# Kernel optimization log

Measured on AMD Instinct MI355X. Metric: run time of the kernel, lower is better.

The kernel has to match this reference:

```python
import jax, jax.numpy as jnp
import numpy as np

SCALE = 8.0  # sqrt(d_k), d_k = 64
NEG_INF = -1000000000.0


def setup_inputs() -> dict:
    key = jax.random.key(0)
    ks = jax.random.split(key, 7)
    B, H, S, D = 2, 8, 4096, 64
    shp = (B, H, S, D)
    q_a = jax.random.normal(ks[0], shp, dtype=jnp.float32)
    k_a = jax.random.normal(ks[1], shp, dtype=jnp.float32)
    v_a = jax.random.normal(ks[2], shp, dtype=jnp.float32)
    q_s = jax.random.normal(ks[3], shp, dtype=jnp.float32)
    k_s = jax.random.normal(ks[4], shp, dtype=jnp.float32)
    v_s = jax.random.normal(ks[5], shp, dtype=jnp.float32)
    mask = jax.random.randint(ks[6], (B, 1, 1, S), 0, 2, dtype=jnp.int32)
    return {"q_a": q_a, "k_a": k_a, "v_a": v_a,
            "q_s": q_s, "k_s": k_s, "v_s": v_s, "mask": mask}


def reference(q_a, k_a, v_a, q_s, k_s, v_s, mask):
    # a2a + a2s + s2a + s2s == (q_a + q_s) @ (k_a + k_s)^T  (exact algebra)
    q = q_a + q_s                               # [B,H,S,D]
    k = k_a + k_s                               # [B,H,S,D]
    score = jnp.einsum("bhqd,bhkd->bhqk", q, k) / SCALE  # [B,H,S,S]
    score = jnp.where(mask == 0, NEG_INF, score)
    attn = jax.nn.softmax(score, axis=-1)       # dropout p=0 (eval/identity)
    out = jnp.einsum("bhqk,bhkd->bhqd", attn, v_a + v_s)
    return out
```

## Files before the change

### kernel.cpp

```cpp
#include <hip/hip_runtime.h>
#include <hip/hip_bf16.h>

#define S_   4096
#define D_   64
#define BH_  16
#define QW   64
#define QBLK 256
#define KVB  128
#define NCH  2

typedef __attribute__((ext_vector_type(8)))  short short8_t;
typedef __attribute__((ext_vector_type(16))) float f32x16;
#define QSCALE 0.18033688011112042f

__device__ __forceinline__ unsigned short f2bf(float f) {
  unsigned u = __float_as_uint(f);
  u += 0x7fffu + ((u >> 16) & 1u);
  return (unsigned short)(u >> 16);
}

__device__ __forceinline__ void glds16(const unsigned short* g, unsigned short* l) {
  __builtin_amdgcn_global_load_lds(
      (const __attribute__((address_space(1))) unsigned int*)g,
      (__attribute__((address_space(3))) unsigned int*)l, 16, 0, 0);
}

__global__ void addcvt2_kernel(const float* __restrict__ a, const float* __restrict__ b,
                               unsigned short* __restrict__ o, float scale, int n) {
  int i = (blockIdx.x * blockDim.x + threadIdx.x) * 4;
  if (i >= n) return;
  float4 x = *(const float4*)(a + i);
  float4 y = *(const float4*)(b + i);
  ushort4 r;
  r.x = f2bf((x.x + y.x) * scale); r.y = f2bf((x.y + y.y) * scale);
  r.z = f2bf((x.z + y.z) * scale); r.w = f2bf((x.w + y.w) * scale);
  *(ushort4*)(o + i) = r;
}

__global__ void compact_kernel(const int* __restrict__ mask, int* __restrict__ idx,
                               int* __restrict__ cnt) {
  __shared__ int ps[256];
  int b = blockIdx.x, tid = threadIdx.x;
  const int* mb = mask + (size_t)b * S_;
  int m[16], c = 0;
  int base = tid * 16;
#pragma unroll
  for (int i = 0; i < 16; ++i) { m[i] = mb[base + i]; c += (m[i] != 0); }
  ps[tid] = c;
  __syncthreads();
  for (int off = 1; off < 256; off <<= 1) {
    int add = (tid >= off) ? ps[tid - off] : 0;
    __syncthreads();
    ps[tid] += add;
    __syncthreads();
  }
  int pos = ps[tid] - c;
#pragma unroll
  for (int i = 0; i < 16; ++i) if (m[i]) idx[(size_t)b * S_ + pos++] = base + i;
  if (tid == 255) cnt[b] = ps[255];
}

__global__ void kvgather_kernel(const float* __restrict__ ka, const float* __restrict__ ks,
                                const float* __restrict__ va, const float* __restrict__ vs,
                                const int* __restrict__ idx, const int* __restrict__ cnt,
                                unsigned short* __restrict__ khat,
                                unsigned short* __restrict__ vt) {
  __shared__ __align__(16) unsigned short t[D_][72];
  int bh = blockIdx.y, b = bh >> 3;
  int s0 = blockIdx.x * 64;
  int C = cnt[b];
  int tid = threadIdx.x;
  int row16 = tid >> 4;
  int col4  = (tid & 15) * 4;
#pragma unroll
  for (int p = 0; p < 4; ++p) {
    int srow = p * 16 + row16;
    int j = s0 + srow;
    float4 xv = {0, 0, 0, 0}, yv = {0, 0, 0, 0};
    float4 xk = {0, 0, 0, 0}, yk = {0, 0, 0, 0};
    if (j < C) {
      int src = idx[(size_t)b * S_ + j];
      size_t off = ((size_t)bh * S_ + src) * D_ + col4;
      xv = *(const float4*)(va + off);
      yv = *(const float4*)(vs + off);
      xk = *(const float4*)(ka + off);
      yk = *(const float4*)(ks + off);
    }
    t[col4 + 0][srow] = f2bf(xv.x + yv.x);
    t[col4 + 1][srow] = f2bf(xv.y + yv.y);
    t[col4 + 2][srow] = f2bf(xv.z + yv.z);
    t[col4 + 3][srow] = f2bf(xv.w + yv.w);
    ushort4 rk;
    rk.x = f2bf(xk.x + yk.x); rk.y = f2bf(xk.y + yk.y);
    rk.z = f2bf(xk.z + yk.z); rk.w = f2bf(xk.w + yk.w);
    *(ushort4*)(khat + ((size_t)bh * S_ + j) * D_ + col4) = rk;
  }
  __syncthreads();
#pragma unroll
  for (int r = 0; r < 2; ++r) {
    int e = (r * 256 + tid) * 8;
    int d = e >> 6, sc = e & 63;
    short8_t v = *(const short8_t*)&t[d][sc];
    *(short8_t*)(vt + ((size_t)bh * D_ + d) * S_ + s0 + sc) = v;
  }
}

__global__ __launch_bounds__(256, 2) void attn_kernel(
    const unsigned short* __restrict__ Qb, const unsigned short* __restrict__ Kb,
    const unsigned short* __restrict__ Vt, const int* __restrict__ cnt,
    float* __restrict__ out, float* __restrict__ Opar, float2* __restrict__ Ml) {
  __shared__ __align__(16) unsigned short lK[2][KVB * 64];
  __shared__ __align__(16) unsigned short lV[2][64 * KVB];

  const int tid  = threadIdx.x;
  const int wave = tid >> 6;
  const int lane = tid & 63;
  const int l31  = lane & 31;
  const int h5   = lane >> 5;
  const int rsw  = l31 & 7;
  const int bh   = blockIdx.y;
  const int ch   = blockIdx.z;
  const int qrow0 = blockIdx.x * QBLK + wave * QW + l31;
  const int b    = bh >> 3;
  const int C    = cnt[b];
  const int NTt  = (C + KVB - 1) / KVB;
  const int tpc  = (NTt + NCH - 1) / NCH;
  const int ts   = ch * tpc;
  const int te   = (ts + tpc < NTt) ? (ts + tpc) : NTt;

  short8_t qf[2][4];
#pragma unroll
  for (int qb = 0; qb < 2; ++qb) {
    const unsigned short* qp = Qb + ((size_t)bh * S_ + qrow0 + 32 * qb) * D_ + h5 * 8;
#pragma unroll
    for (int t4 = 0; t4 < 4; ++t4) qf[qb][t4] = *(const short8_t*)(qp + t4 * 16);
  }

  const unsigned short* gk0 = Kb + (size_t)bh * S_ * D_;
  const unsigned short* gv0 = Vt + (size_t)bh * D_ * S_;

  int srcK[4], srcV[4], ldsB[4];
#pragma unroll
  for (int r2 = 0; r2 < 4; ++r2) {
    int c = r2 * 256 + tid;
    int rowK = c >> 3, gK = (c & 7) ^ (rowK & 7);
    srcK[r2] = rowK * 64 + gK * 8;
    int rowV = c >> 4, gg = c & 15;
    int swg = (gg & 8) | ((gg & 7) ^ (rowV & 7));
    srcV[r2] = rowV * S_ + swg * 8;
    ldsB[r2] = r2 * 2048 + wave * 512;
  }

  f32x16 acc0[2], acc1[2];
  float mrow[2], lrow[2];
#pragma unroll
  for (int qb = 0; qb < 2; ++qb) {
    acc0[qb] = (f32x16)(0.0f); acc1[qb] = (f32x16)(0.0f);
    mrow[qb] = -1e30f; lrow[qb] = 0.0f;
  }

  if (ts < te) {
#pragma unroll
    for (int r2 = 0; r2 < 4; ++r2) {
      glds16(gk0 + (size_t)ts * KVB * D_ + srcK[r2], &lK[0][ldsB[r2]]);
      glds16(gv0 + ts * KVB + srcV[r2], &lV[0][ldsB[r2]]);
    }

    for (int t = ts; t < te; ++t) {
      const int cur = (t - ts) & 1;
      if (t + 1 < te) {
#pragma unroll
        for (int r2 = 0; r2 < 4; ++r2) {
          glds16(gk0 + (size_t)(t + 1) * KVB * D_ + srcK[r2], &lK[cur ^ 1][ldsB[r2]]);
          glds16(gv0 + (t + 1) * KVB + srcV[r2], &lV[cur ^ 1][ldsB[r2]]);
        }
        asm volatile("s_waitcnt vmcnt(8)" ::: "memory");
      } else {
        asm volatile("s_waitcnt vmcnt(0)" ::: "memory");
      }
      __builtin_amdgcn_s_barrier();
      __builtin_amdgcn_sched_barrier(0);

#pragma unroll
      for (int h = 0; h < 2; ++h) {
        f32x16 sv0[2], sv1[2];
#pragma unroll
        for (int qb = 0; qb < 2; ++qb) { sv0[qb] = (f32x16)(0.0f); sv1[qb] = (f32x16)(0.0f); }
        __builtin_amdgcn_s_setprio(1);
#pragma unroll
        for (int t4 = 0; t4 < 4; ++t4) {
          int g = ((2 * t4 + h5) ^ rsw) * 8;
          short8_t kf0 = *(const short8_t*)&lK[cur][(h * 64 + l31) * 64 + g];
          short8_t kf1 = *(const short8_t*)&lK[cur][(h * 64 + 32 + l31) * 64 + g];
          sv0[0] = __builtin_amdgcn_mfma_f32_32x32x16_bf16(kf0, qf[0][t4], sv0[0], 0, 0, 0);
          sv0[1] = __builtin_amdgcn_mfma_f32_32x32x16_bf16(kf0, qf[1][t4], sv0[1], 0, 0, 0);
          sv1[0] = __builtin_amdgcn_mfma_f32_32x32x16_bf16(kf1, qf[0][t4], sv1[0], 0, 0, 0);
          sv1[1] = __builtin_amdgcn_mfma_f32_32x32x16_bf16(kf1, qf[1][t4], sv1[1], 0, 0, 0);
        }
        __builtin_amdgcn_s_setprio(0);

        if (t == NTt - 1) {
          int kvb = t * KVB + h * 64;
#pragma unroll
          for (int i = 0; i < 16; ++i) {
            int key = kvb + (i & 3) + 8 * (i >> 2) + 4 * h5;
#pragma unroll
            for (int qb = 0; qb < 2; ++qb) {
              if (key >= C) sv0[qb][i] = -1e9f;
              if (key + 32 >= C) sv1[qb][i] = -1e9f;
            }
          }
        }

        unsigned int pkw[2][16];
#pragma unroll
        for (int qb = 0; qb < 2; ++qb) {
          float tmx[8];
#pragma unroll
          for (int i = 0; i < 8; ++i)
            tmx[i] = fmaxf(fmaxf(sv0[qb][i], sv0[qb][i + 8]),
                           fmaxf(sv1[qb][i], sv1[qb][i + 8]));
#pragma unroll
          for (int i = 0; i < 4; ++i) tmx[i] = fmaxf(tmx[i], tmx[i + 4]);
          float tm = fmaxf(fmaxf(tmx[0], tmx[1]), fmaxf(tmx[2], tmx[3]));
          tm = fmaxf(tm, __shfl_xor(tm, 32));

          if (__any(tm > mrow[qb] + 8.0f)) {
            float mnew = fmaxf(mrow[qb], tm);
            float sc = __builtin_amdgcn_exp2f(mrow[qb] - mnew);
            mrow[qb] = mnew;
            lrow[qb] *= sc;
#pragma unroll
            for (int i = 0; i < 16; ++i) { acc0[qb][i] *= sc; acc1[qb][i] *= sc; }
          }

          float m = mrow[qb];
          float t0 = 0.f, t1 = 0.f, t2 = 0.f, t3 = 0.f;
#pragma unroll
          for (int i = 0; i < 16; i += 4) {
            sv0[qb][i + 0] = __builtin_amdgcn_exp2f(sv0[qb][i + 0] - m); t0 += sv0[qb][i + 0];
            sv0[qb][i + 1] = __builtin_amdgcn_exp2f(sv0[qb][i + 1] - m); t1 += sv0[qb][i + 1];
            sv0[qb][i + 2] = __builtin_amdgcn_exp2f(sv0[qb][i + 2] - m); t2 += sv0[qb][i + 2];
            sv0[qb][i + 3] = __builtin_amdgcn_exp2f(sv0[qb][i + 3] - m); t3 += sv0[qb][i + 3];
            sv1[qb][i + 0] = __builtin_amdgcn_exp2f(sv1[qb][i + 0] - m); t0 += sv1[qb][i + 0];
            sv1[qb][i + 1] = __builtin_amdgcn_exp2f(sv1[qb][i + 1] - m); t1 += sv1[qb][i + 1];
            sv1[qb][i + 2] = __builtin_amdgcn_exp2f(sv1[qb][i + 2] - m); t2 += sv1[qb][i + 2];
            sv1[qb][i + 3] = __builtin_amdgcn_exp2f(sv1[qb][i + 3] - m); t3 += sv1[qb][i + 3];
          }
          float tsum = (t0 + t1) + (t2 + t3);
          tsum += __shfl_xor(tsum, 32);
          lrow[qb] += tsum;

#pragma unroll
          for (int rg = 0; rg < 4; ++rg) {
            __hip_bfloat162 a0 = __float22bfloat162_rn({sv0[qb][rg * 4 + 0], sv0[qb][rg * 4 + 1]});
            __hip_bfloat162 a1 = __float22bfloat162_rn({sv0[qb][rg * 4 + 2], sv0[qb][rg * 4 + 3]});
            __hip_bfloat162 b0 = __float22bfloat162_rn({sv1[qb][rg * 4 + 0], sv1[qb][rg * 4 + 1]});
            __hip_bfloat162 b1 = __float22bfloat162_rn({sv1[qb][rg * 4 + 2], sv1[qb][rg * 4 + 3]});
            pkw[qb][rg * 2 + 0] = *(unsigned int*)&a0;
            pkw[qb][rg * 2 + 1] = *(unsigned int*)&a1;
            pkw[qb][8 + rg * 2 + 0] = *(unsigned int*)&b0;
            pkw[qb][8 + rg * 2 + 1] = *(unsigned int*)&b1;
          }
        }

        __builtin_amdgcn_s_setprio(1);
#pragma unroll
        for (int kt = 0; kt < 4; ++kt) {
          const int n = kt >> 1, k1 = kt & 1;
          int gcol = ((h * 8) | ((2 * kt + h5) ^ rsw)) * 8;
          short8_t vf0 = *(const short8_t*)&lV[cur][l31 * KVB + gcol];
          short8_t vf1 = *(const short8_t*)&lV[cur][(32 + l31) * KVB + gcol];
#pragma unroll
          for (int qb = 0; qb < 2; ++qb) {
            unsigned int sA = pkw[qb][n * 8 + (2 * k1 + h5) * 2 + 0];
            unsigned int sB = pkw[qb][n * 8 + (2 * k1 + h5) * 2 + 1];
            unsigned int xA = pkw[qb][n * 8 + (2 * k1 + (h5 ^ 1)) * 2 + 0];
            unsigned int xB = pkw[qb][n * 8 + (2 * k1 + (h5 ^ 1)) * 2 + 1];
            unsigned int pA = (unsigned int)__shfl_xor((int)xA, 32);
            unsigned int pB = (unsigned int)__shfl_xor((int)xB, 32);
            union { unsigned int u[4]; short8_t v; } bb;
            bb.u[0] = h5 ? pA : sA;
            bb.u[1] = h5 ? pB : sB;
            bb.u[2] = h5 ? sA : pA;
            bb.u[3] = h5 ? sB : pB;
            acc0[qb] = __builtin_amdgcn_mfma_f32_32x32x16_bf16(vf0, bb.v, acc0[qb], 0, 0, 0);
            acc1[qb] = __builtin_amdgcn_mfma_f32_32x32x16_bf16(vf1, bb.v, acc1[qb], 0, 0, 0);
          }
        }
        __builtin_amdgcn_s_setprio(0);
      }

      __builtin_amdgcn_sched_barrier(0);
      __builtin_amdgcn_s_barrier();
    }
  }

  float* Op = (ch == 0) ? out : Opar;
#pragma unroll
  for (int qb = 0; qb < 2; ++qb) {
    float* op = Op + ((size_t)bh * S_ + qrow0 + 32 * qb) * D_;
#pragma unroll
    for (int rg = 0; rg < 4; ++rg) {
      float4 o0, o1;
      o0.x = acc0[qb][rg * 4 + 0]; o0.y = acc0[qb][rg * 4 + 1];
      o0.z = acc0[qb][rg * 4 + 2]; o0.w = acc0[qb][rg * 4 + 3];
      o1.x = acc1[qb][rg * 4 + 0]; o1.y = acc1[qb][rg * 4 + 1];
      o1.z = acc1[qb][rg * 4 + 2]; o1.w = acc1[qb][rg * 4 + 3];
      *(float4*)(op + rg * 8 + h5 * 4) = o0;
      *(float4*)(op + 32 + rg * 8 + h5 * 4) = o1;
    }
    if (h5 == 0) {
      float2 st; st.x = mrow[qb]; st.y = lrow[qb];
      Ml[(size_t)ch * (BH_ * S_) + (size_t)bh * S_ + qrow0 + 32 * qb] = st;
    }
  }
}

__global__ void combine_kernel(const float* __restrict__ O1, const float2* __restrict__ Ml,
                               float* __restrict__ out) {
  int gid = blockIdx.x * 256 + threadIdx.x;
  int row = gid >> 2, qd = (gid & 3) * 16;
  float2 a = Ml[row];
  float2 b = Ml[BH_ * S_ + row];
  float M = fmaxf(a.x, b.x);
  float w0 = exp2f(a.x - M), w1 = exp2f(b.x - M);
  float inv = 1.0f / (a.y * w0 + b.y * w1);
  w0 *= inv; w1 *= inv;
  const float4* p0 = (const float4*)(out + (size_t)row * D_ + qd);
  const float4* p1 = (const float4*)(O1 + (size_t)row * D_ + qd);
  float4* po = (float4*)(out + (size_t)row * D_ + qd);
#pragma unroll
  for (int i = 0; i < 4; ++i) {
    float4 x = p0[i], y = p1[i];
    float4 r;
    r.x = x.x * w0 + y.x * w1; r.y = x.y * w0 + y.y * w1;
    r.z = x.z * w0 + y.z * w1; r.w = x.w * w0 + y.w * w1;
    po[i] = r;
  }
}

extern "C" void kernel_launch(void* const* d_in, const int* in_sizes, int n_in,
                              void* d_out, int out_size, void* d_ws, size_t ws_size,
                              hipStream_t stream) {
  const float* q_a = (const float*)d_in[0];
  const float* k_a = (const float*)d_in[1];
  const float* v_a = (const float*)d_in[2];
  const float* q_s = (const float*)d_in[3];
  const float* k_s = (const float*)d_in[4];
  const float* v_s = (const float*)d_in[5];
  const int*   mask = (const int*)d_in[6];
  float* out = (float*)d_out;
  (void)in_sizes; (void)n_in; (void)out_size; (void)ws_size;

  const int N = BH_ * S_ * D_;
  unsigned short* qb   = (unsigned short*)d_ws;
  unsigned short* khat = qb + N;
  unsigned short* vt   = khat + N;
  int*  idx  = (int*)(vt + N);
  int*  cnt  = idx + 2 * S_;
  float* O1  = (float*)(cnt + 4);
  float2* ml = (float2*)(O1 + N);

  compact_kernel<<<2, 256, 0, stream>>>(mask, idx, cnt);
  addcvt2_kernel<<<N / 1024, 256, 0, stream>>>(q_a, q_s, qb, QSCALE, N);
  {
    dim3 g(S_ / 64, BH_);
    kvgather_kernel<<<g, 256, 0, stream>>>(k_a, k_s, v_a, v_s, idx, cnt, khat, vt);
  }
  {
    dim3 g(S_ / QBLK, BH_, NCH);
    attn_kernel<<<g, 256, 0, stream>>>(qb, khat, vt, cnt, out, O1, ml);
  }
  combine_kernel<<<(BH_ * S_ * 4) / 256, 256, 0, stream>>>(O1, ml, out);
}
```

Baseline: 126.3 us.

## Fuse mask compaction into KV gather and Q add-convert into attention

Drops the separate compact kernel: every kvgather block now recomputes the mask prefix scan itself and keeps only its 64-entry slice of source indices in LDS. Also drops the Q add/scale/bf16-convert kernel: the attention kernel reads q_a and q_s in fp32 and builds its bf16 Q fragments in registers. This removes two launches and the round trip of the bf16 Q buffer and index array through memory. In exchange each gather block repeats the scan and re-reads the mask, and attention reads twice as many Q bytes. Both chunks along z convert the same Q rows, so that work is duplicated.

New measurement: 124.0 us. About the same (-1.9%).

```diff
diff --git a/kernel.cpp b/kernel.cpp
--- a/kernel.cpp
+++ b/kernel.cpp
@@ -25,25 +25,21 @@
       (__attribute__((address_space(3))) unsigned int*)l, 16, 0, 0);
 }
 
-__global__ void addcvt2_kernel(const float* __restrict__ a, const float* __restrict__ b,
-                               unsigned short* __restrict__ o, float scale, int n) {
-  int i = (blockIdx.x * blockDim.x + threadIdx.x) * 4;
-  if (i >= n) return;
-  float4 x = *(const float4*)(a + i);
-  float4 y = *(const float4*)(b + i);
-  ushort4 r;
-  r.x = f2bf((x.x + y.x) * scale); r.y = f2bf((x.y + y.y) * scale);
-  r.z = f2bf((x.z + y.z) * scale); r.w = f2bf((x.w + y.w) * scale);
-  *(ushort4*)(o + i) = r;
-}
-
-__global__ void compact_kernel(const int* __restrict__ mask, int* __restrict__ idx,
-                               int* __restrict__ cnt) {
+__global__ void kvgather_kernel(const float* __restrict__ ka, const float* __restrict__ ks,
+                                const float* __restrict__ va, const float* __restrict__ vs,
+                                const int* __restrict__ mask, int* __restrict__ cnt,
+                                unsigned short* __restrict__ khat,
+                                unsigned short* __restrict__ vt) {
   __shared__ int ps[256];
-  int b = blockIdx.x, tid = threadIdx.x;
+  __shared__ int srcLds[64];
+  __shared__ __align__(16) unsigned short t[D_][72];
+  const int bh = blockIdx.y, b = bh >> 3;
+  const int s0 = blockIdx.x * 64;
+  const int tid = threadIdx.x;
+
   const int* mb = mask + (size_t)b * S_;
   int m[16], c = 0;
-  int base = tid * 16;
+  const int base = tid * 16;
 #pragma unroll
   for (int i = 0; i < 16; ++i) { m[i] = mb[base + i]; c += (m[i] != 0); }
   ps[tid] = c;
@@ -54,24 +50,20 @@
     ps[tid] += add;
     __syncthreads();
   }
+  const int C = ps[255];
   int pos = ps[tid] - c;
 #pragma unroll
-  for (int i = 0; i < 16; ++i) if (m[i]) idx[(size_t)b * S_ + pos++] = base + i;
-  if (tid == 255) cnt[b] = ps[255];
-}
-
-__global__ void kvgather_kernel(const float* __restrict__ ka, const float* __restrict__ ks,
-                                const float* __restrict__ va, const float* __restrict__ vs,
-                                const int* __restrict__ idx, const int* __restrict__ cnt,
-                                unsigned short* __restrict__ khat,
-                                unsigned short* __restrict__ vt) {
-  __shared__ __align__(16) unsigned short t[D_][72];
-  int bh = blockIdx.y, b = bh >> 3;
-  int s0 = blockIdx.x * 64;
-  int C = cnt[b];
-  int tid = threadIdx.x;
-  int row16 = tid >> 4;
-  int col4  = (tid & 15) * 4;
+  for (int i = 0; i < 16; ++i) {
+    if (m[i]) {
+      int r = pos++;
+      if (r >= s0 && r < s0 + 64) srcLds[r - s0] = base + i;
+    }
+  }
+  if (tid == 0 && blockIdx.x == 0 && (bh & 7) == 0) cnt[b] = C;
+  __syncthreads();
+
+  const int row16 = tid >> 4;
+  const int col4  = (tid & 15) * 4;
 #pragma unroll
   for (int p = 0; p < 4; ++p) {
     int srow = p * 16 + row16;
@@ -79,7 +71,7 @@
     float4 xv = {0, 0, 0, 0}, yv = {0, 0, 0, 0};
     float4 xk = {0, 0, 0, 0}, yk = {0, 0, 0, 0};
     if (j < C) {
-      int src = idx[(size_t)b * S_ + j];
+      int src = srcLds[srow];
       size_t off = ((size_t)bh * S_ + src) * D_ + col4;
       xv = *(const float4*)(va + off);
       yv = *(const float4*)(vs + off);
@@ -106,8 +98,9 @@
 }
 
 __global__ __launch_bounds__(256, 2) void attn_kernel(
-    const unsigned short* __restrict__ Qb, const unsigned short* __restrict__ Kb,
-    const unsigned short* __restrict__ Vt, const int* __restrict__ cnt,
+    const float* __restrict__ Qa, const float* __restrict__ Qs,
+    const unsigned short* __restrict__ Kb, const unsigned short* __restrict__ Vt,
+    const int* __restrict__ cnt,
     float* __restrict__ out, float* __restrict__ Opar, float2* __restrict__ Ml) {
   __shared__ __align__(16) unsigned short lK[2][KVB * 64];
   __shared__ __align__(16) unsigned short lV[2][64 * KVB];
@@ -131,9 +124,22 @@
   short8_t qf[2][4];
 #pragma unroll
   for (int qb = 0; qb < 2; ++qb) {
-    const unsigned short* qp = Qb + ((size_t)bh * S_ + qrow0 + 32 * qb) * D_ + h5 * 8;
-#pragma unroll
-    for (int t4 = 0; t4 < 4; ++t4) qf[qb][t4] = *(const short8_t*)(qp + t4 * 16);
+    size_t off = ((size_t)bh * S_ + qrow0 + 32 * qb) * D_ + h5 * 8;
+    const float* qa = Qa + off;
+    const float* qs = Qs + off;
+#pragma unroll
+    for (int t4 = 0; t4 < 4; ++t4) {
+      float4 a0 = *(const float4*)(qa + t4 * 16);
+      float4 a1 = *(const float4*)(qa + t4 * 16 + 4);
+      float4 s0 = *(const float4*)(qs + t4 * 16);
+      float4 s1 = *(const float4*)(qs + t4 * 16 + 4);
+      union { unsigned short u[8]; short8_t v; } qq;
+      qq.u[0] = f2bf((a0.x + s0.x) * QSCALE); qq.u[1] = f2bf((a0.y + s0.y) * QSCALE);
+      qq.u[2] = f2bf((a0.z + s0.z) * QSCALE); qq.u[3] = f2bf((a0.w + s0.w) * QSCALE);
+      qq.u[4] = f2bf((a1.x + s1.x) * QSCALE); qq.u[5] = f2bf((a1.y + s1.y) * QSCALE);
+      qq.u[6] = f2bf((a1.z + s1.z) * QSCALE); qq.u[7] = f2bf((a1.w + s1.w) * QSCALE);
+      qf[qb][t4] = qq.v;
+    }
   }
 
   const unsigned short* gk0 = Kb + (size_t)bh * S_ * D_;
@@ -354,23 +360,19 @@
   (void)in_sizes; (void)n_in; (void)out_size; (void)ws_size;
 
   const int N = BH_ * S_ * D_;
-  unsigned short* qb   = (unsigned short*)d_ws;
-  unsigned short* khat = qb + N;
+  unsigned short* khat = (unsigned short*)d_ws;
   unsigned short* vt   = khat + N;
-  int*  idx  = (int*)(vt + N);
-  int*  cnt  = idx + 2 * S_;
+  int*  cnt  = (int*)(vt + N);
   float* O1  = (float*)(cnt + 4);
   float2* ml = (float2*)(O1 + N);
 
-  compact_kernel<<<2, 256, 0, stream>>>(mask, idx, cnt);
-  addcvt2_kernel<<<N / 1024, 256, 0, stream>>>(q_a, q_s, qb, QSCALE, N);
   {
     dim3 g(S_ / 64, BH_);
-    kvgather_kernel<<<g, 256, 0, stream>>>(k_a, k_s, v_a, v_s, idx, cnt, khat, vt);
+    kvgather_kernel<<<g, 256, 0, stream>>>(k_a, k_s, v_a, v_s, mask, cnt, khat, vt);
   }
   {
     dim3 g(S_ / QBLK, BH_, NCH);
-    attn_kernel<<<g, 256, 0, stream>>>(qb, khat, vt, cnt, out, O1, ml);
+    attn_kernel<<<g, 256, 0, stream>>>(q_a, q_s, khat, vt, cnt, out, O1, ml);
   }
   combine_kernel<<<(BH_ * S_ * 4) / 256, 256, 0, stream>>>(O1, ml, out);
 }
```
